# Kernel tuning notes

Hardware: AMD Instinct MI355X
Metric: run time of the kernel (lower is better)

Reference implementation:

```python
import jax, jax.numpy as jnp
import numpy as np

N = 10000      # nodes
E = 160000     # edges (before self loops)
F_IN = 512     # in_features
F_OUT = 256    # out_features
SLOPE = 0.2    # LeakyReLU negative slope (PyG GATConv default)
EPS = 1e-12    # F.normalize eps


def setup_inputs() -> dict:
    key = jax.random.key(0)
    ks = jax.random.split(key, 14)
    feat = jax.random.normal(ks[0], (N, F_IN), jnp.float32)
    feat_a = jax.random.normal(ks[1], (N, F_IN), jnp.float32)
    edge_index = jax.random.randint(ks[2], (2, E), 0, N, dtype=jnp.int32)
    # binary neighborhood mask; diagonal set so every row has >=1 entry
    gn = (jax.random.uniform(ks[3], (N, N)) < 0.0016).astype(jnp.float32)
    graph_neigh = gn.at[jnp.arange(N), jnp.arange(N)].set(1.0)
    s1 = 1.0 / np.sqrt(F_IN)
    s2 = 1.0 / np.sqrt(F_OUT)
    return {
        "feat": feat,
        "feat_a": feat_a,
        "edge_index": edge_index,
        "graph_neigh": graph_neigh,
        # conv1: GATConv(F_IN -> F_OUT, heads=1)
        "W1": jax.random.normal(ks[4], (F_OUT, F_IN), jnp.float32) * s1,
        "att_src1": jax.random.normal(ks[5], (F_OUT,), jnp.float32) * s2,
        "att_dst1": jax.random.normal(ks[6], (F_OUT,), jnp.float32) * s2,
        "b1": jnp.zeros((F_OUT,), jnp.float32),
        # conv2: GATConv(F_OUT -> F_IN, heads=1)
        "W2": jax.random.normal(ks[7], (F_IN, F_OUT), jnp.float32) * s2,
        "att_src2": jax.random.normal(ks[8], (F_IN,), jnp.float32) * s1,
        "att_dst2": jax.random.normal(ks[9], (F_IN,), jnp.float32) * s1,
        "b2": jnp.zeros((F_IN,), jnp.float32),
        # discriminator bilinear
        "Wd": jax.random.normal(ks[10], (F_OUT, F_OUT), jnp.float32) * s2,
        "bd": jnp.zeros((), jnp.float32),
    }


def _gat_conv(x, src, dst, W, a_src, a_dst, b):
    # PyG GATConv, heads=1, concat=True, add_self_loops already applied.
    h = x @ W.T                       # [N, out]
    a_s = h @ a_src                   # [N]
    a_d = h @ a_dst                   # [N]
    e = a_s[src] + a_d[dst]           # [E+N]
    e = jnp.where(e > 0, e, SLOPE * e)  # leaky relu
    m = jax.ops.segment_max(e, dst, num_segments=N)
    p = jnp.exp(e - m[dst])
    s = jax.ops.segment_sum(p, dst, num_segments=N)
    coef = p / s[dst]                 # per-dst softmax over incoming edges
    out = jax.ops.segment_sum(coef[:, None] * h[src], dst, num_segments=N)
    return out + b


def reference(feat, feat_a, edge_index, graph_neigh, W1, att_src1, att_dst1, b1,
              W2, att_src2, att_dst2, b2, Wd, bd):
    loops = jnp.arange(N, dtype=edge_index.dtype)
    src = jnp.concatenate([edge_index[0], loops])
    dst = jnp.concatenate([edge_index[1], loops])

    z = _gat_conv(feat, src, dst, W1, att_src1, att_dst1, b1)      # [N, F_OUT]
    hiden_emb = z
    h = _gat_conv(z, src, dst, W2, att_src2, att_dst2, b2)         # [N, F_IN]
    emb = jax.nn.relu(z)
    z_a = _gat_conv(feat_a, src, dst, W1, att_src1, att_dst1, b1)
    emb_a = jax.nn.relu(z_a)

    def readout(e):
        vsum = graph_neigh @ e                                     # [N, F_OUT]
        row_sum = graph_neigh.sum(axis=1, keepdims=True)
        g = vsum / row_sum
        g = g / jnp.maximum(jnp.linalg.norm(g, axis=1, keepdims=True), EPS)
        return jax.nn.sigmoid(g)

    g = readout(emb)
    g_a = readout(emb_a)

    def bilin(x1, x2):
        return jnp.einsum('nd,de,ne->n', x1, Wd, x2)[:, None] + bd

    ret = jnp.concatenate([bilin(emb, g), bilin(emb_a, g)], axis=1)      # [N, 2]
    ret_a = jnp.concatenate([bilin(emb_a, g_a), bilin(emb, g_a)], axis=1)
    return (hiden_emb, h, ret, ret_a)
```

## Files before the change

kernel.cpp:

```cpp
#include <hip/hip_runtime.h>


#define N_NODES 10000
#define F_IN    512
#define F_OUT   256
#define SLOPE   0.2f
#define BCAP    64

typedef unsigned short ushort_t;
typedef __attribute__((ext_vector_type(8))) short short8;
typedef __attribute__((ext_vector_type(4))) float f32x4;

__device__ __forceinline__ float bf2f(ushort_t h) {
    union { unsigned u; float f; } v;
    v.u = ((unsigned)h) << 16;
    return v.f;
}
__device__ __forceinline__ ushort_t f2bf(float f) {
    union { float f; unsigned u; } v; v.f = f;
    unsigned r = v.u + 0x7FFFu + ((v.u >> 16) & 1u);
    return (ushort_t)(r >> 16);
}

#define NF (N_NODES * 512)
#define NW1 (512 * 256)
#define NW2 (512 * 256)
#define NWD (256 * 256)

__global__ __launch_bounds__(256) void cvt_all(const float* __restrict__ feat,
                                               const float* __restrict__ feat_a,
                                               const float* __restrict__ W1,
                                               const float* __restrict__ W2,
                                               const float* __restrict__ Wd,
                                               ushort_t* __restrict__ featbf,
                                               ushort_t* __restrict__ W1bf,
                                               ushort_t* __restrict__ W2bf,
                                               ushort_t* __restrict__ Wdbf,
                                               uint4* __restrict__ zbase, int zu4) {
    int q = blockIdx.x * 256 + threadIdx.x;
    const int total = (2 * NF + NW1 + NW2 + NWD) / 4;
    if (q >= total) {
        int zi = q - total;
        if (zi < zu4) zbase[zi] = make_uint4(0, 0, 0, 0);
        return;
    }
    int i = q * 4;
    const float* s; ushort_t* d;
    if (i < NF)               { s = feat   + i;                 d = featbf + i; }
    else if (i < 2 * NF)      { s = feat_a + (i - NF);          d = featbf + i; }
    else if (i < 2 * NF + NW1){ s = W1 + (i - 2 * NF);          d = W1bf + (i - 2 * NF); }
    else if (i < 2 * NF + NW1 + NW2) { s = W2 + (i - 2 * NF - NW1); d = W2bf + (i - 2 * NF - NW1); }
    else                      { s = Wd + (i - 2 * NF - NW1 - NW2); d = Wdbf + (i - 2 * NF - NW1 - NW2); }
    float4 v = *(const float4*)s;
    uint2 r;
    r.x = (unsigned)f2bf(v.x) | ((unsigned)f2bf(v.y) << 16);
    r.y = (unsigned)f2bf(v.z) | ((unsigned)f2bf(v.w) << 16);
    *(uint2*)d = r;
}

#define BM 64
#define BN 64
#define BK 32
#define MT1 157
#define MT2 313

__device__ __forceinline__ void gemm_bt_dev(ushort_t* As, ushort_t* Bs,
        int bx, int by,
        const ushort_t* __restrict__ A, const ushort_t* __restrict__ B,
        ushort_t* __restrict__ C, int M, int Nn, int K,
        const float* __restrict__ asrc, const float* __restrict__ adst,
        float* __restrict__ as_out, float* __restrict__ ad_out) {
    int m0 = bx * BM;
    int n0 = by * BN;
    int tid = threadIdx.x;
    int wave = tid >> 6, lane = tid & 63;
    int quad = lane >> 4, r16 = lane & 15;

    f32x4 acc[4] = {};

    int srow = tid >> 2;
    int schunk = tid & 3;
    int a_row = m0 + srow; if (a_row >= M) a_row = M - 1;
    const uint4* Ag = (const uint4*)(A + (size_t)a_row * K);
    const uint4* Bg = (const uint4*)(B + (size_t)(n0 + srow) * K);
    int s_sw = srow * BK + ((schunk ^ (srow & 3)) * 8);

    for (int k0 = 0; k0 < K; k0 += BK) {
        uint4 av = Ag[(k0 >> 3) + schunk];
        uint4 bv = Bg[(k0 >> 3) + schunk];
        __syncthreads();
        *(uint4*)&As[s_sw] = av;
        *(uint4*)&Bs[s_sw] = bv;
        __syncthreads();
        int am = wave * 16 + r16;
        short8 a = *(const short8*)&As[am * BK + ((quad ^ (am & 3)) * 8)];
#pragma unroll
        for (int i = 0; i < 4; i++) {
            int bn = i * 16 + r16;
            short8 b = *(const short8*)&Bs[bn * BK + ((quad ^ (bn & 3)) * 8)];
            acc[i] = __builtin_amdgcn_mfma_f32_16x16x32_bf16(a, b, acc[i], 0, 0, 0);
        }
    }
    int m_base = m0 + wave * 16 + quad * 4;
#pragma unroll
    for (int i = 0; i < 4; i++) {
        int n = n0 + i * 16 + r16;
#pragma unroll
        for (int r = 0; r < 4; r++) {
            int m = m_base + r;
            if (m < M) C[(size_t)m * Nn + n] = f2bf(acc[i][r]);
        }
    }
    if (as_out) {
        float a0 = asrc[n0 + r16],      d0 = adst[n0 + r16];
        float a1 = asrc[n0 + 16 + r16], d1 = adst[n0 + 16 + r16];
        float a2 = asrc[n0 + 32 + r16], d2 = adst[n0 + 32 + r16];
        float a3 = asrc[n0 + 48 + r16], d3 = adst[n0 + 48 + r16];
#pragma unroll
        for (int r = 0; r < 4; r++) {
            float s  = acc[0][r] * a0 + acc[1][r] * a1 + acc[2][r] * a2 + acc[3][r] * a3;
            float dd = acc[0][r] * d0 + acc[1][r] * d1 + acc[2][r] * d2 + acc[3][r] * d3;
#pragma unroll
            for (int off = 1; off < 16; off <<= 1) {
                s  += __shfl_xor(s, off);
                dd += __shfl_xor(dd, off);
            }
            int m = m_base + r;
            if (r16 == 0 && m < M) {
                atomicAdd(&as_out[m], s);
                atomicAdd(&ad_out[m], dd);
            }
        }
    }
}

template<int NV>
__device__ __forceinline__ void accum_row(float wgt, const ushort_t* p, float* acc) {
    if constexpr (NV == 4) {
        uint2 u = *(const uint2*)p;
        acc[0] += wgt * bf2f((ushort_t)(u.x & 0xFFFFu));
        acc[1] += wgt * bf2f((ushort_t)(u.x >> 16));
        acc[2] += wgt * bf2f((ushort_t)(u.y & 0xFFFFu));
        acc[3] += wgt * bf2f((ushort_t)(u.y >> 16));
    } else {
        uint4 u = *(const uint4*)p;
        acc[0] += wgt * bf2f((ushort_t)(u.x & 0xFFFFu));
        acc[1] += wgt * bf2f((ushort_t)(u.x >> 16));
        acc[2] += wgt * bf2f((ushort_t)(u.y & 0xFFFFu));
        acc[3] += wgt * bf2f((ushort_t)(u.y >> 16));
        acc[4] += wgt * bf2f((ushort_t)(u.z & 0xFFFFu));
        acc[5] += wgt * bf2f((ushort_t)(u.z >> 16));
        acc[6] += wgt * bf2f((ushort_t)(u.w & 0xFFFFu));
        acc[7] += wgt * bf2f((ushort_t)(u.w >> 16));
    }
}

template<int NV>
__device__ __forceinline__ void store_bf(ushort_t* dst, const float* z, bool relu) {
    unsigned rp[NV / 2];
#pragma unroll
    for (int k = 0; k < NV; k += 2) {
        float x = relu ? fmaxf(z[k], 0.f) : z[k];
        float y = relu ? fmaxf(z[k + 1], 0.f) : z[k + 1];
        rp[k / 2] = (unsigned)f2bf(x) | ((unsigned)f2bf(y) << 16);
    }
    if constexpr (NV == 4) {
        *(uint2*)dst = make_uint2(rp[0], rp[1]);
    } else {
        *(uint4*)dst = make_uint4(rp[0], rp[1], rp[2], rp[3]);
    }
}

template<int FF>
__device__ __forceinline__ void row_conv_dev(int w,
        const int* __restrict__ cnt, const int* __restrict__ buckets,
        const float* __restrict__ a_s, const float* __restrict__ a_d,
        const ushort_t* __restrict__ h, const float* __restrict__ bias,
        int nfirst,
        float* __restrict__ out0, ushort_t* __restrict__ outZ,
        ushort_t* __restrict__ outB, ushort_t* __restrict__ out1) {
    constexpr int NV = FF / 64;
    int lane = threadIdx.x & 63;
    int sel = (w >= nfirst) ? 1 : 0;
    int n = w - sel * nfirst;
    size_t roff = (size_t)sel * (size_t)nfirst;
    int deg = min(cnt[n], BCAP);
    float adn = a_d[roff + n];

    float acc[NV];
#pragma unroll
    for (int k = 0; k < NV; k++) acc[k] = 0.f;

    int cv = 0; float e = -1e30f;
    if (lane < deg) {
        cv = buckets[n * BCAP + lane];
        float t = a_s[roff + cv] + adn;
        e = t > 0.f ? t : SLOPE * t;
    }
    float m = e;
#pragma unroll
    for (int off = 32; off; off >>= 1) m = fmaxf(m, __shfl_xor(m, off));
    float wv = (lane < deg) ? expf(e - m) : 0.f;
    float ls = wv;
#pragma unroll
    for (int off = 32; off; off >>= 1) ls += __shfl_xor(ls, off);
    float inv_s = ls > 0.f ? 1.f / ls : 0.f;
    int j = 0;
    for (; j + 3 < deg; j += 4) {
        float w0 = __shfl(wv, j),     w1 = __shfl(wv, j + 1);
        float w2 = __shfl(wv, j + 2), w3 = __shfl(wv, j + 3);
        int   q0 = __shfl(cv, j),     q1 = __shfl(cv, j + 1);
        int   q2 = __shfl(cv, j + 2), q3 = __shfl(cv, j + 3);
        accum_row<NV>(w0, h + (size_t)(roff + q0) * FF + lane * NV, acc);
        accum_row<NV>(w1, h + (size_t)(roff + q1) * FF + lane * NV, acc);
        accum_row<NV>(w2, h + (size_t)(roff + q2) * FF + lane * NV, acc);
        accum_row<NV>(w3, h + (size_t)(roff + q3) * FF + lane * NV, acc);
    }
    for (; j < deg; j++) {
        float wj = __shfl(wv, j);
        int   qj = __shfl(cv, j);
        accum_row<NV>(wj, h + (size_t)(roff + qj) * FF + lane * NV, acc);
    }

    float z[NV];
#pragma unroll
    for (int k = 0; k < NV; k++) z[k] = acc[k] * inv_s + bias[lane * NV + k];

    size_t obase = (size_t)n * FF + lane * NV;
    if (sel == 0) {
        if (out0) {
#pragma unroll
            for (int k = 0; k < NV; k += 4)
                *(float4*)(out0 + obase + k) = make_float4(z[k], z[k+1], z[k+2], z[k+3]);
        }
        if (outZ) store_bf<NV>(outZ + obase, z, false);
        if (outB) store_bf<NV>(outB + obase, z, true);
    } else {
        if (out1) store_bf<NV>(out1 + obase, z, true);
    }
}

template<int FF>
__global__ __launch_bounds__(256) void row_conv_w(const int* __restrict__ cnt,
                                                  const int* __restrict__ buckets,
                                                  const float* __restrict__ a_s,
                                                  const float* __restrict__ a_d,
                                                  const ushort_t* __restrict__ h,
                                                  const float* __restrict__ bias,
                                                  int nfirst, int ntot,
                                                  float* __restrict__ out0,
                                                  ushort_t* __restrict__ outZ,
                                                  ushort_t* __restrict__ outB,
                                                  ushort_t* __restrict__ out1) {
    int w = blockIdx.x * 4 + (threadIdx.x >> 6);
    if (w >= ntot) return;
    row_conv_dev<FF>(w, cnt, buckets, a_s, a_d, h, bias, nfirst, out0, outZ, outB, out1);
}

#define RCAP 256

__device__ __forceinline__ void readout_dev(int nbase, char* smemraw,
        const float* __restrict__ gn,
        const ushort_t* __restrict__ embB, const ushort_t* __restrict__ embA,
        ushort_t* __restrict__ g, ushort_t* __restrict__ ga) {
    int wid = threadIdx.x >> 6, lane = threadIdx.x & 63;
    int n = nbase + wid;
    int (*lists)[RCAP] = (int(*)[RCAP])smemraw;
    int* cnts = (int*)(smemraw + 4 * RCAP * 4);
    if (lane == 0) cnts[wid] = 0;
    __syncthreads();
    const uint4* rowp = (const uint4*)(gn + (size_t)n * N_NODES);
    const int NU4 = N_NODES / 4;
    for (int idx = lane; idx < NU4; idx += 64) {
        uint4 v = rowp[idx];
        if (v.x & 0x7FFFFFFFu) { int p = atomicAdd(&cnts[wid], 1); if (p < RCAP) lists[wid][p] = idx * 4; }
        if (v.y & 0x7FFFFFFFu) { int p = atomicAdd(&cnts[wid], 1); if (p < RCAP) lists[wid][p] = idx * 4 + 1; }
        if (v.z & 0x7FFFFFFFu) { int p = atomicAdd(&cnts[wid], 1); if (p < RCAP) lists[wid][p] = idx * 4 + 2; }
        if (v.w & 0x7FFFFFFFu) { int p = atomicAdd(&cnts[wid], 1); if (p < RCAP) lists[wid][p] = idx * 4 + 3; }
    }
    __syncthreads();
    int c = min(cnts[wid], RCAP);
    float a0[4] = {}, a1[4] = {};
    int j = 0;
    for (; j + 3 < c; j += 4) {
        int i0 = lists[wid][j],     i1 = lists[wid][j + 1];
        int i2 = lists[wid][j + 2], i3 = lists[wid][j + 3];
        accum_row<4>(1.f, embB + (size_t)i0 * 256 + lane * 4, a0);
        accum_row<4>(1.f, embB + (size_t)i1 * 256 + lane * 4, a0);
        accum_row<4>(1.f, embB + (size_t)i2 * 256 + lane * 4, a0);
        accum_row<4>(1.f, embB + (size_t)i3 * 256 + lane * 4, a0);
        accum_row<4>(1.f, embA + (size_t)i0 * 256 + lane * 4, a1);
        accum_row<4>(1.f, embA + (size_t)i1 * 256 + lane * 4, a1);
        accum_row<4>(1.f, embA + (size_t)i2 * 256 + lane * 4, a1);
        accum_row<4>(1.f, embA + (size_t)i3 * 256 + lane * 4, a1);
    }
    for (; j < c; j++) {
        int node = lists[wid][j];
        accum_row<4>(1.f, embB + (size_t)node * 256 + lane * 4, a0);
        accum_row<4>(1.f, embA + (size_t)node * 256 + lane * 4, a1);
    }
    float inv = 1.f / (float)(c > 0 ? c : 1);
    float u0[4], u1[4];
    float s0 = 0.f, s1 = 0.f;
#pragma unroll
    for (int k = 0; k < 4; k++) {
        u0[k] = a0[k] * inv; s0 += u0[k] * u0[k];
        u1[k] = a1[k] * inv; s1 += u1[k] * u1[k];
    }
#pragma unroll
    for (int off = 32; off; off >>= 1) {
        s0 += __shfl_xor(s0, off);
        s1 += __shfl_xor(s1, off);
    }
    float r0 = 1.f / fmaxf(sqrtf(s0), 1e-12f);
    float r1 = 1.f / fmaxf(sqrtf(s1), 1e-12f);
    float go[4], gao[4];
#pragma unroll
    for (int k = 0; k < 4; k++) {
        go[k]  = 1.f / (1.f + expf(-u0[k] * r0));
        gao[k] = 1.f / (1.f + expf(-u1[k] * r1));
    }
    store_bf<4>(g  + (size_t)n * 256 + lane * 4, go,  false);
    store_bf<4>(ga + (size_t)n * 256 + lane * 4, gao, false);
}

#define G1B (MT2 * 4)

__global__ __launch_bounds__(256) void k_conv1(const ushort_t* __restrict__ featbf,
                                               const ushort_t* __restrict__ W1bf,
                                               ushort_t* __restrict__ h1cat,
                                               const float* __restrict__ asrc1,
                                               const float* __restrict__ adst1,
                                               float* __restrict__ as1cat,
                                               float* __restrict__ ad1cat,
                                               const int* __restrict__ src,
                                               const int* __restrict__ dst,
                                               int E, int* cnt, int* buckets) {
    __shared__ __align__(16) ushort_t As[BM * BK];
    __shared__ __align__(16) ushort_t Bs[BN * BK];
    int b = blockIdx.x;
    if (b < G1B) {
        gemm_bt_dev(As, Bs, b % MT2, b / MT2, featbf, W1bf, h1cat,
                    2 * N_NODES, F_OUT, F_IN, asrc1, adst1, as1cat, ad1cat);
    } else {
        int i = (b - G1B) * 256 + (int)threadIdx.x;
        if (i < E) {
            int d = dst[i];
            d = d < 0 ? 0 : (d >= N_NODES ? N_NODES - 1 : d);
            int s = src[i];
            s = s < 0 ? 0 : (s >= N_NODES ? N_NODES - 1 : s);
            int p = atomicAdd(&cnt[d], 1);
            if (p < BCAP) buckets[d * BCAP + p] = s;
        } else if (i < E + N_NODES) {
            int v = i - E;
            int p = atomicAdd(&cnt[v], 1);
            if (p < BCAP) buckets[v * BCAP + p] = v;
        }
    }
}

#define RO_BLOCKS 2500
#define G2B (MT1 * 8)

__global__ __launch_bounds__(256) void k_stage2(const ushort_t* __restrict__ zbf,
                                                const ushort_t* __restrict__ W2bf,
                                                ushort_t* __restrict__ h2,
                                                const float* __restrict__ asrc2,
                                                const float* __restrict__ adst2,
                                                float* __restrict__ as2,
                                                float* __restrict__ ad2,
                                                const float* __restrict__ gn,
                                                const ushort_t* __restrict__ embB,
                                                const ushort_t* __restrict__ embA,
                                                ushort_t* __restrict__ g,
                                                ushort_t* __restrict__ ga) {
    __shared__ __align__(16) char smem[2 * BM * BK * 2];
    int b = blockIdx.x;
    if (b < RO_BLOCKS) {
        readout_dev(b * 4, smem, gn, embB, embA, g, ga);
    } else {
        int bb = b - RO_BLOCKS;
        gemm_bt_dev((ushort_t*)smem, (ushort_t*)smem + BM * BK, bb % MT1, bb / MT1,
                    zbf, W2bf, h2, N_NODES, F_IN, F_OUT, asrc2, adst2, as2, ad2);
    }
}

__global__ __launch_bounds__(256) void k_stage3(const int* __restrict__ cnt,
                                                const int* __restrict__ buckets,
                                                const float* __restrict__ as2,
                                                const float* __restrict__ ad2,
                                                const ushort_t* __restrict__ h2,
                                                const float* __restrict__ b2,
                                                float* __restrict__ out_h,
                                                const ushort_t* __restrict__ Gcat,
                                                const ushort_t* __restrict__ Wdbf,
                                                ushort_t* __restrict__ R2) {
    __shared__ __align__(16) ushort_t As[BM * BK];
    __shared__ __align__(16) ushort_t Bs[BN * BK];
    int b = blockIdx.x;
    if (b < RO_BLOCKS) {
        int w = b * 4 + ((int)threadIdx.x >> 6);
        row_conv_dev<512>(w, cnt, buckets, as2, ad2, h2, b2, N_NODES,
                          out_h, nullptr, nullptr, nullptr);
    } else {
        int bb = b - RO_BLOCKS;
        gemm_bt_dev(As, Bs, bb % MT2, bb / MT2, Gcat, Wdbf, R2,
                    2 * N_NODES, 256, 256, nullptr, nullptr, nullptr, nullptr);
    }
}

__global__ __launch_bounds__(256) void bilin_kernel(const float* __restrict__ z,
                                                    const ushort_t* __restrict__ embA,
                                                    const ushort_t* __restrict__ Q,
                                                    const ushort_t* __restrict__ Qa,
                                                    const float* __restrict__ bdp,
                                                    float* __restrict__ ret,
                                                    float* __restrict__ ret_a) {
    int row = blockIdx.x * 4 + (threadIdx.x >> 6);
    int lane = threadIdx.x & 63;
    if (row >= N_NODES) return;
    const float*    zr = z    + (size_t)row * 256;
    const ushort_t* er = embA + (size_t)row * 256;
    const ushort_t* q  = Q    + (size_t)row * 256;
    const ushort_t* qa = Qa   + (size_t)row * 256;
    float d00 = 0, d01 = 0, d10 = 0, d11 = 0;
    for (int d = lane; d < 256; d += 64) {
        float em = fmaxf(zr[d], 0.f);
        float ea = bf2f(er[d]);
        float qv = bf2f(q[d]), qav = bf2f(qa[d]);
        d00 += em * qv;
        d01 += ea * qv;
        d10 += ea * qav;
        d11 += em * qav;
    }
    for (int off = 32; off; off >>= 1) {
        d00 += __shfl_down(d00, off);
        d01 += __shfl_down(d01, off);
        d10 += __shfl_down(d10, off);
        d11 += __shfl_down(d11, off);
    }
    if (lane == 0) {
        float bd = bdp[0];
        ret[row * 2]       = d00 + bd;
        ret[row * 2 + 1]   = d01 + bd;
        ret_a[row * 2]     = d10 + bd;
        ret_a[row * 2 + 1] = d11 + bd;
    }
}

extern "C" void kernel_launch(void* const* d_in, const int* in_sizes, int n_in,
                              void* d_out, int out_size, void* d_ws, size_t ws_size,
                              hipStream_t stream) {
    const float* feat    = (const float*)d_in[0];
    const float* feat_a  = (const float*)d_in[1];
    const int*   eidx    = (const int*)d_in[2];
    const float* gn      = (const float*)d_in[3];
    const float* W1      = (const float*)d_in[4];
    const float* asrc1   = (const float*)d_in[5];
    const float* adst1   = (const float*)d_in[6];
    const float* b1      = (const float*)d_in[7];
    const float* W2      = (const float*)d_in[8];
    const float* asrc2   = (const float*)d_in[9];
    const float* adst2   = (const float*)d_in[10];
    const float* b2      = (const float*)d_in[11];
    const float* Wd      = (const float*)d_in[12];
    const float* bd      = (const float*)d_in[13];

    const int N = N_NODES;
    const int E = in_sizes[2] / 2;
    const int* src = eidx;
    const int* dst = eidx + E;

    float* out_z    = (float*)d_out;
    float* out_h    = out_z + (size_t)N * F_OUT;
    float* out_ret  = out_h + (size_t)N * F_IN;
    float* out_reta = out_ret + (size_t)N * 2;

    size_t off = 0;
    char* wsb = (char*)d_ws;
    auto carve = [&](size_t bytes) -> void* {
        void* p = wsb + off;
        off = (off + bytes + 255) & ~(size_t)255;
        return p;
    };
    ushort_t* R1     = (ushort_t*)carve((size_t)2 * N * 256 * 2);
    ushort_t* R2     = (ushort_t*)carve((size_t)2 * N * 256 * 2);
    ushort_t* Gcat   = (ushort_t*)carve((size_t)2 * N * 256 * 2);
    ushort_t* embA   = (ushort_t*)carve((size_t)N * 256 * 2);
    ushort_t* embB   = (ushort_t*)carve((size_t)N * 256 * 2);
    ushort_t* zbf    = (ushort_t*)carve((size_t)N * 256 * 2);
    ushort_t* featbf = (ushort_t*)carve((size_t)2 * N * 512 * 2);
    ushort_t* W1bf   = (ushort_t*)carve((size_t)NW1 * 2);
    ushort_t* W2bf   = (ushort_t*)carve((size_t)NW2 * 2);
    ushort_t* Wdbf   = (ushort_t*)carve((size_t)NWD * 2);
    size_t zstart = off;
    float* as1cat = (float*)carve((size_t)2 * N * 4);
    float* ad1cat = (float*)carve((size_t)2 * N * 4);
    float* as2    = (float*)carve((size_t)N * 4);
    float* ad2    = (float*)carve((size_t)N * 4);
    int*   cnt    = (int*)carve((size_t)N * 4);
    size_t zend = off;
    int*   buckets = (int*)carve((size_t)N * BCAP * 4);

    ushort_t* h1cat = R1;
    ushort_t* h2    = R1;
    ushort_t* Qb    = R2;
    ushort_t* Qab   = R2 + (size_t)N * 256;

    const int cvt_total = (2 * NF + NW1 + NW2 + NWD) / 4;
    const int zu4 = (int)((zend - zstart) / 16);
    cvt_all<<<(cvt_total + zu4 + 255) / 256, 256, 0, stream>>>(
        feat, feat_a, W1, W2, Wd, featbf, W1bf, W2bf, Wdbf,
        (uint4*)(wsb + zstart), zu4);

    const int bucketBlocks = (E + N + 255) / 256;
    k_conv1<<<G1B + bucketBlocks, 256, 0, stream>>>(featbf, W1bf, h1cat,
                                                    asrc1, adst1, as1cat, ad1cat,
                                                    src, dst, E, cnt, buckets);

    row_conv_w<256><<<2 * N / 4, 256, 0, stream>>>(cnt, buckets, as1cat, ad1cat, h1cat, b1,
                                                   N, 2 * N, out_z, zbf, embB, embA);

    k_stage2<<<RO_BLOCKS + G2B, 256, 0, stream>>>(zbf, W2bf, h2, asrc2, adst2, as2, ad2,
                                                  gn, embB, embA, Gcat, Gcat + (size_t)N * 256);

    k_stage3<<<RO_BLOCKS + G1B, 256, 0, stream>>>(cnt, buckets, as2, ad2, h2, b2, out_h,
                                                  Gcat, Wdbf, R2);

    bilin_kernel<<<(N + 3) / 4, 256, 0, stream>>>(out_z, embA, Qb, Qab, bd, out_ret, out_reta);
}
```

Measured before the change: 683.3 us.

## Precompute graph_neigh bitmask in conv1 kernel and scan bits in readout

Adds a mask-building phase to the conv1 launch that compresses the dense 10000x10000 fp32 neighbourhood matrix into a per-row 64-bit ballot bitmask. The readout then walks set bits with ctz instead of rescanning the full dense row. The intent is to move the 400MB dense scan off the critical stage2 path so it overlaps with the conv1 GEMM, and to make readout list-building cheap. The dense matrix is still read once, the mask costs extra workspace (about 12.8MB), and conv1 gets longer.

Measured after the change: 688.0 us. Within noise of the previous version (+0.7%).

```diff
diff --git a/kernel.cpp b/kernel.cpp
--- a/kernel.cpp
+++ b/kernel.cpp
@@ -257,10 +257,50 @@
     row_conv_dev<FF>(w, cnt, buckets, a_s, a_d, h, bias, nfirst, out0, outZ, outB, out1);
 }
 
+#define NSEG  40
+#define MWPR  160
+#define NTASK (N_NODES * NSEG)
+#define CMP_BLOCKS 2048
+
+__device__ __forceinline__ void mask_build_dev(int cb, const unsigned* __restrict__ gnu,
+                                               unsigned long long* __restrict__ mask) {
+    int wvid = cb * 4 + ((int)threadIdx.x >> 6);
+    int lane = threadIdx.x & 63;
+    const int NWAVE = CMP_BLOCKS * 4;
+    for (int tbase = wvid * 4; tbase < NTASK; tbase += NWAVE * 4) {
+        uint4 u[4]; int row[4], seg[4]; bool ok[4];
+#pragma unroll
+        for (int q = 0; q < 4; q++) {
+            int t = tbase + q;
+            ok[q] = t < NTASK;
+            int tt = ok[q] ? t : 0;
+            row[q] = tt / NSEG;
+            seg[q] = tt - row[q] * NSEG;
+            int col = seg[q] * 256 + lane * 4;
+            if (ok[q] && col < N_NODES)
+                u[q] = *(const uint4*)(gnu + (size_t)row[q] * N_NODES + col);
+            else
+                u[q] = make_uint4(0, 0, 0, 0);
+        }
+#pragma unroll
+        for (int q = 0; q < 4; q++) {
+            unsigned long long b0 = __ballot((u[q].x & 0x7FFFFFFFu) != 0u);
+            unsigned long long b1 = __ballot((u[q].y & 0x7FFFFFFFu) != 0u);
+            unsigned long long b2 = __ballot((u[q].z & 0x7FFFFFFFu) != 0u);
+            unsigned long long b3 = __ballot((u[q].w & 0x7FFFFFFFu) != 0u);
+            if (ok[q] && lane < 4) {
+                unsigned long long mv = lane == 0 ? b0 : lane == 1 ? b1
+                                      : lane == 2 ? b2 : b3;
+                mask[(size_t)row[q] * MWPR + seg[q] * 4 + lane] = mv;
+            }
+        }
+    }
+}
+
 #define RCAP 256
 
 __device__ __forceinline__ void readout_dev(int nbase, char* smemraw,
-        const float* __restrict__ gn,
+        const unsigned long long* __restrict__ mask,
         const ushort_t* __restrict__ embB, const ushort_t* __restrict__ embA,
         ushort_t* __restrict__ g, ushort_t* __restrict__ ga) {
     int wid = threadIdx.x >> 6, lane = threadIdx.x & 63;
@@ -269,14 +309,16 @@
     int* cnts = (int*)(smemraw + 4 * RCAP * 4);
     if (lane == 0) cnts[wid] = 0;
     __syncthreads();
-    const uint4* rowp = (const uint4*)(gn + (size_t)n * N_NODES);
-    const int NU4 = N_NODES / 4;
-    for (int idx = lane; idx < NU4; idx += 64) {
-        uint4 v = rowp[idx];
-        if (v.x & 0x7FFFFFFFu) { int p = atomicAdd(&cnts[wid], 1); if (p < RCAP) lists[wid][p] = idx * 4; }
-        if (v.y & 0x7FFFFFFFu) { int p = atomicAdd(&cnts[wid], 1); if (p < RCAP) lists[wid][p] = idx * 4 + 1; }
-        if (v.z & 0x7FFFFFFFu) { int p = atomicAdd(&cnts[wid], 1); if (p < RCAP) lists[wid][p] = idx * 4 + 2; }
-        if (v.w & 0x7FFFFFFFu) { int p = atomicAdd(&cnts[wid], 1); if (p < RCAP) lists[wid][p] = idx * 4 + 3; }
+    const unsigned long long* mrow = mask + (size_t)n * MWPR;
+    for (int widx = lane; widx < MWPR; widx += 64) {
+        unsigned long long w = mrow[widx];
+        int base = widx << 6;
+        while (w) {
+            int b = (int)__builtin_ctzll(w);
+            w &= w - 1;
+            int p = atomicAdd(&cnts[wid], 1);
+            if (p < RCAP) lists[wid][p] = base + b;
+        }
     }
     __syncthreads();
     int c = min(cnts[wid], RCAP);
@@ -335,15 +377,19 @@
                                                float* __restrict__ ad1cat,
                                                const int* __restrict__ src,
                                                const int* __restrict__ dst,
-                                               int E, int* cnt, int* buckets) {
+                                               int E, int* cnt, int* buckets,
+                                               const unsigned* __restrict__ gnu,
+                                               unsigned long long* __restrict__ mask) {
     __shared__ __align__(16) ushort_t As[BM * BK];
     __shared__ __align__(16) ushort_t Bs[BN * BK];
     int b = blockIdx.x;
     if (b < G1B) {
         gemm_bt_dev(As, Bs, b % MT2, b / MT2, featbf, W1bf, h1cat,
                     2 * N_NODES, F_OUT, F_IN, asrc1, adst1, as1cat, ad1cat);
+    } else if (b < G1B + CMP_BLOCKS) {
+        mask_build_dev(b - G1B, gnu, mask);
     } else {
-        int i = (b - G1B) * 256 + (int)threadIdx.x;
+        int i = (b - G1B - CMP_BLOCKS) * 256 + (int)threadIdx.x;
         if (i < E) {
             int d = dst[i];
             d = d < 0 ? 0 : (d >= N_NODES ? N_NODES - 1 : d);
@@ -369,7 +415,7 @@
                                                 const float* __restrict__ adst2,
                                                 float* __restrict__ as2,
                                                 float* __restrict__ ad2,
-                                                const float* __restrict__ gn,
+                                                const unsigned long long* __restrict__ mask,
                                                 const ushort_t* __restrict__ embB,
                                                 const ushort_t* __restrict__ embA,
                                                 ushort_t* __restrict__ g,
@@ -377,7 +423,7 @@
     __shared__ __align__(16) char smem[2 * BM * BK * 2];
     int b = blockIdx.x;
     if (b < RO_BLOCKS) {
-        readout_dev(b * 4, smem, gn, embB, embA, g, ga);
+        readout_dev(b * 4, smem, mask, embB, embA, g, ga);
     } else {
         int bb = b - RO_BLOCKS;
         gemm_bt_dev((ushort_t*)smem, (ushort_t*)smem + BM * BK, bb % MT1, bb / MT1,
@@ -493,6 +539,7 @@
     ushort_t* W1bf   = (ushort_t*)carve((size_t)NW1 * 2);
     ushort_t* W2bf   = (ushort_t*)carve((size_t)NW2 * 2);
     ushort_t* Wdbf   = (ushort_t*)carve((size_t)NWD * 2);
+    unsigned long long* mask = (unsigned long long*)carve((size_t)N * MWPR * 8);
     size_t zstart = off;
     float* as1cat = (float*)carve((size_t)2 * N * 4);
     float* ad1cat = (float*)carve((size_t)2 * N * 4);
@@ -514,15 +561,15 @@
         (uint4*)(wsb + zstart), zu4);
 
     const int bucketBlocks = (E + N + 255) / 256;
-    k_conv1<<<G1B + bucketBlocks, 256, 0, stream>>>(featbf, W1bf, h1cat,
-                                                    asrc1, adst1, as1cat, ad1cat,
-                                                    src, dst, E, cnt, buckets);
+    k_conv1<<<G1B + CMP_BLOCKS + bucketBlocks, 256, 0, stream>>>(
+        featbf, W1bf, h1cat, asrc1, adst1, as1cat, ad1cat,
+        src, dst, E, cnt, buckets, (const unsigned*)gn, mask);
 
     row_conv_w<256><<<2 * N / 4, 256, 0, stream>>>(cnt, buckets, as1cat, ad1cat, h1cat, b1,
                                                    N, 2 * N, out_z, zbf, embB, embA);
 
     k_stage2<<<RO_BLOCKS + G2B, 256, 0, stream>>>(zbf, W2bf, h2, asrc2, adst2, as2, ad2,
-                                                  gn, embB, embA, Gcat, Gcat + (size_t)N * 256);
+                                                  mask, embB, embA, Gcat, Gcat + (size_t)N * 256);
 
     k_stage3<<<RO_BLOCKS + G1B, 256, 0, stream>>>(cnt, buckets, as2, ad2, h2, b2, out_h,
                                                   Gcat, Wdbf, R2);
```
